# Performance work log

Measured on AMD Instinct MI355X. Metric: run time of the kernel, lower is better.

## Reference

```python
import jax, jax.numpy as jnp
import numpy as np

N_NODES = 100000
N_EDGES = 1600000
IN_DIM = 256
OUT_DIM = 32


def setup_inputs() -> dict:
    key = jax.random.key(0)
    k1, k2, k3, k4, k5 = jax.random.split(key, 5)
    x = jax.random.normal(k1, (N_NODES, IN_DIM), dtype=jnp.float32)
    src = jax.random.randint(k2, (N_EDGES,), 0, N_NODES, dtype=jnp.int32)
    dst = jax.random.randint(k3, (N_EDGES,), 0, N_NODES, dtype=jnp.int32)
    # GraphConv parameters (DGL: weight [in, out], bias [out])
    W = jax.random.normal(k4, (IN_DIM, OUT_DIM), dtype=jnp.float32) / np.sqrt(IN_DIM)
    b = jnp.zeros((OUT_DIM,), dtype=jnp.float32)
    return {"x": x, "src": src, "dst": dst, "W": W, "b": b}


def reference(x, src, dst, W, b):
    # DGL GraphConv, norm='both', allow_zero_in_degree=True:
    #   out = D_in^{-1/2} A D_out^{-1/2} X W + b  (degrees clamped to min 1)
    ones = jnp.ones(src.shape[0], dtype=x.dtype)
    deg_out = jax.ops.segment_sum(ones, src, num_segments=N_NODES)
    deg_in = jax.ops.segment_sum(ones, dst, num_segments=N_NODES)
    norm_src = jnp.clip(deg_out, 1.0, None) ** -0.5  # [N]
    norm_dst = jnp.clip(deg_in, 1.0, None) ** -0.5   # [N]
    # in_dim > out_dim: project first (smaller messages), then aggregate
    h = (x * norm_src[:, None]) @ W                  # [N, out]
    msgs = h[src]                                    # [E, out] gather
    agg = jax.ops.segment_sum(msgs, dst, num_segments=N_NODES)  # [N, out]
    return agg * norm_dst[:, None] + b
```

## Files before the change

### kernel.cpp

```cpp
#include <hip/hip_runtime.h>

#define N_NODES 100000
#define N_EDGES 1600000
#define IN_DIM 256
#define OUT_DIM 32

#define SB_SHIFT 7
#define NSB ((N_NODES + 127) >> 7)
#define SBCAP 2368
#define NB1 782
#define NGB ((N_NODES + 255) / 256)
#define NI4 (N_EDGES / 4)

typedef __attribute__((ext_vector_type(8))) short short8;
typedef __attribute__((ext_vector_type(16))) float f32x16;

#define WT_STRIDE 264

__device__ inline unsigned short f2bf(float f) {
    unsigned u = __float_as_uint(f);
    unsigned r = u + 0x7FFF + ((u >> 16) & 1);
    return (unsigned short)(r >> 16);
}
__device__ inline float bf2f(unsigned short us) {
    return __uint_as_float((unsigned)us << 16);
}

__global__ __launch_bounds__(512) void k_mega(const int* __restrict__ src,
                                              const int* __restrict__ dst,
                                              unsigned long long* __restrict__ qcnt,
                                              unsigned* __restrict__ gsb,
                                              unsigned char* __restrict__ gss,
                                              const float* __restrict__ x,
                                              const float* __restrict__ W,
                                              unsigned short* __restrict__ h2) {
    __shared__ __align__(16) int smemI[6 * NSB];
    const int tid = threadIdx.x;
    const int bid = blockIdx.x;
    const int g = bid / 3;
    const int rem = bid - g * 3;

    if (rem == 0) {
        unsigned short* WT = (unsigned short*)smemI;
        #pragma unroll
        for (int i = 0; i < 16; ++i) {
            int idx = tid + i * 512;
            WT[(idx & 31) * WT_STRIDE + (idx >> 5)] = f2bf(W[idx]);
        }
        __syncthreads();

        const int wv = tid >> 6;
        const int lane = tid & 63;
        const int col = lane & 31;
        const int hi = lane >> 5;

        const int row0 = g * 256 + wv * 32;
        int grow = row0 + col;
        int growc = grow < N_NODES ? grow : N_NODES - 1;
        const float4* xrow = reinterpret_cast<const float4*>(x + (size_t)growc * IN_DIM);

        f32x16 acc = {0.f,0.f,0.f,0.f,0.f,0.f,0.f,0.f,
                      0.f,0.f,0.f,0.f,0.f,0.f,0.f,0.f};

        #pragma unroll 4
        for (int t = 0; t < 16; ++t) {
            int k4 = t * 4 + hi * 2;
            float4 p0 = xrow[k4];
            float4 p1 = xrow[k4 + 1];
            short8 a;
            a[0] = (short)f2bf(p0.x); a[1] = (short)f2bf(p0.y);
            a[2] = (short)f2bf(p0.z); a[3] = (short)f2bf(p0.w);
            a[4] = (short)f2bf(p1.x); a[5] = (short)f2bf(p1.y);
            a[6] = (short)f2bf(p1.z); a[7] = (short)f2bf(p1.w);
            short8 bfr = *reinterpret_cast<const short8*>(
                &WT[col * WT_STRIDE + t * 16 + hi * 8]);
            acc = __builtin_amdgcn_mfma_f32_32x32x16_bf16(a, bfr, acc, 0, 0, 0);
        }

        #pragma unroll
        for (int r = 0; r < 16; ++r) {
            int rowi = (r & 3) + 8 * (r >> 2) + 4 * hi;
            int go = row0 + rowi;
            if (go < N_NODES)
                h2[(size_t)go * OUT_DIM + col] = f2bf(acc[r]);
        }
    } else {
        const int pb = 2 * g + rem - 1;
        int* histD = smemI;
        int* bbD   = smemI + NSB;
        int* curD  = smemI + 2 * NSB;
        int* histS = smemI + 3 * NSB;
        int* bbS   = smemI + 4 * NSB;
        int* curS  = smemI + 5 * NSB;

        for (int i = tid; i < NSB; i += 512) {
            histD[i] = 0; curD[i] = 0; histS[i] = 0; curS[i] = 0;
        }
        __syncthreads();

        const int gid = pb * 512 + tid;
        const bool valid = gid < NI4;
        int4 sv, dv;
        if (valid) {
            sv = reinterpret_cast<const int4*>(src)[gid];
            dv = reinterpret_cast<const int4*>(dst)[gid];
            atomicAdd(&histD[dv.x >> SB_SHIFT], 1);
            atomicAdd(&histD[dv.y >> SB_SHIFT], 1);
            atomicAdd(&histD[dv.z >> SB_SHIFT], 1);
            atomicAdd(&histD[dv.w >> SB_SHIFT], 1);
            atomicAdd(&histS[sv.x >> SB_SHIFT], 1);
            atomicAdd(&histS[sv.y >> SB_SHIFT], 1);
            atomicAdd(&histS[sv.z >> SB_SHIFT], 1);
            atomicAdd(&histS[sv.w >> SB_SHIFT], 1);
        }
        __syncthreads();

        for (int i = tid; i < NSB; i += 512) {
            unsigned long long pack =
                ((unsigned long long)(unsigned)histS[i] << 32) | (unsigned)histD[i];
            unsigned long long old = atomicAdd(&qcnt[i], pack);
            bbD[i] = (int)(old & 0xFFFFFFFFull);
            bbS[i] = (int)(old >> 32);
        }
        __syncthreads();

        if (valid) {
            int ss[4] = {sv.x, sv.y, sv.z, sv.w};
            int dd[4] = {dv.x, dv.y, dv.z, dv.w};
            #pragma unroll
            for (int u = 0; u < 4; ++u) {
                int d = dd[u], s = ss[u];
                int r = d >> SB_SHIFT;
                int lp = atomicAdd(&curD[r], 1);
                int pos = bbD[r] + lp;
                if (pos < SBCAP)
                    gsb[(size_t)r * SBCAP + pos] =
                        ((unsigned)(d & 127) << 17) | (unsigned)s;
                int rs = s >> SB_SHIFT;
                int lp2 = atomicAdd(&curS[rs], 1);
                int pos2 = bbS[rs] + lp2;
                if (pos2 < SBCAP)
                    gss[(size_t)rs * SBCAP + pos2] = (unsigned char)(s & 127);
            }
        }
    }
}

__global__ __launch_bounds__(256) void k_deg2(const int* __restrict__ qcnt2,
                                              const unsigned char* __restrict__ gss,
                                              float* __restrict__ nrmtab) {
    __shared__ int hist[128];
    const int r = blockIdx.x;
    const int tid = threadIdx.x;
    if (tid < 128) hist[tid] = 0;
    __syncthreads();
    int cnt = qcnt2[2 * r + 1];
    if (cnt > SBCAP) cnt = SBCAP;
    const unsigned char* bp = gss + (size_t)r * SBCAP;
    for (int i = tid; i < cnt; i += 256)
        atomicAdd(&hist[bp[i]], 1);
    __syncthreads();
    if (tid < 128) {
        int nn = (r << SB_SHIFT) + tid;
        if (nn < N_NODES) {
            int dg = hist[tid];
            nrmtab[nn] = rsqrtf((float)(dg > 1 ? dg : 1));
        }
    }
}

__global__ __launch_bounds__(512) void k_combo2(const int* __restrict__ qcnt2,
                                                const unsigned* __restrict__ gsb,
                                                const unsigned short* __restrict__ h2,
                                                const float* __restrict__ nrmtab,
                                                const float* __restrict__ bias,
                                                float* __restrict__ out) {
    __shared__ unsigned pstage[SBCAP];
    __shared__ int esl[SBCAP];
    __shared__ int hist[128];
    __shared__ int pref[128];
    __shared__ int cur[128];

    const int r = blockIdx.x;
    const int tid = threadIdx.x;

    if (tid < 128) { hist[tid] = 0; cur[tid] = 0; }
    int cnt = qcnt2[2 * r];
    if (cnt > SBCAP) cnt = SBCAP;
    const unsigned* bp = gsb + (size_t)r * SBCAP;
    __syncthreads();

    for (int i = tid; i < cnt; i += 512) {
        unsigned pay = bp[i];
        pstage[i] = pay;
        atomicAdd(&hist[pay >> 17], 1);
    }
    __syncthreads();

    int v = 0;
    if (tid < 128) { v = hist[tid]; pref[tid] = v; }
    __syncthreads();
    #pragma unroll
    for (int off = 1; off < 128; off <<= 1) {
        int t = (tid < 128 && tid >= off) ? pref[tid - off] : 0;
        __syncthreads();
        if (tid < 128) pref[tid] += t;
        __syncthreads();
    }
    if (tid < 128) pref[tid] -= v;
    __syncthreads();

    for (int i = tid; i < cnt; i += 512) {
        unsigned pay = pstage[i];
        int l = (int)(pay >> 17);
        int lp = atomicAdd(&cur[l], 1);
        esl[pref[l] + lp] = (int)(pay & 0x1FFFF);
    }
    __syncthreads();

    const int q = tid & 7;
    const int nl = tid >> 3;
    const float4 bb = reinterpret_cast<const float4*>(bias)[q];
    #pragma unroll
    for (int sweep = 0; sweep < 2; ++sweep) {
        int l = sweep * 64 + nl;
        int st = pref[l];
        int deg = hist[l];
        float4 acc = make_float4(0.f, 0.f, 0.f, 0.f);
        int j = 0;
        for (; j + 4 <= deg; j += 4) {
            int s0 = esl[st + j + 0];
            int s1 = esl[st + j + 1];
            int s2 = esl[st + j + 2];
            int s3 = esl[st + j + 3];
            float w0 = nrmtab[s0];
            float w1 = nrmtab[s1];
            float w2 = nrmtab[s2];
            float w3 = nrmtab[s3];
            ushort4 a0 = *reinterpret_cast<const ushort4*>(&h2[(size_t)s0 * OUT_DIM + q * 4]);
            ushort4 a1 = *reinterpret_cast<const ushort4*>(&h2[(size_t)s1 * OUT_DIM + q * 4]);
            ushort4 a2 = *reinterpret_cast<const ushort4*>(&h2[(size_t)s2 * OUT_DIM + q * 4]);
            ushort4 a3 = *reinterpret_cast<const ushort4*>(&h2[(size_t)s3 * OUT_DIM + q * 4]);
            acc.x += bf2f(a0.x) * w0 + bf2f(a1.x) * w1 + bf2f(a2.x) * w2 + bf2f(a3.x) * w3;
            acc.y += bf2f(a0.y) * w0 + bf2f(a1.y) * w1 + bf2f(a2.y) * w2 + bf2f(a3.y) * w3;
            acc.z += bf2f(a0.z) * w0 + bf2f(a1.z) * w1 + bf2f(a2.z) * w2 + bf2f(a3.z) * w3;
            acc.w += bf2f(a0.w) * w0 + bf2f(a1.w) * w1 + bf2f(a2.w) * w2 + bf2f(a3.w) * w3;
        }
        for (; j < deg; ++j) {
            int s = esl[st + j];
            float w = nrmtab[s];
            ushort4 a = *reinterpret_cast<const ushort4*>(&h2[(size_t)s * OUT_DIM + q * 4]);
            acc.x += bf2f(a.x) * w; acc.y += bf2f(a.y) * w;
            acc.z += bf2f(a.z) * w; acc.w += bf2f(a.w) * w;
        }
        int node = (r << SB_SHIFT) + l;
        if (node < N_NODES) {
            float nrm = rsqrtf((float)(deg > 1 ? deg : 1));
            float4 o = make_float4(acc.x * nrm + bb.x, acc.y * nrm + bb.y,
                                   acc.z * nrm + bb.z, acc.w * nrm + bb.w);
            reinterpret_cast<float4*>(out)[(size_t)node * 8 + q] = o;
        }
    }
}

extern "C" void kernel_launch(void* const* d_in, const int* in_sizes, int n_in,
                              void* d_out, int out_size, void* d_ws, size_t ws_size,
                              hipStream_t stream) {
    const float* x   = (const float*)d_in[0];
    const int*   src = (const int*)d_in[1];
    const int*   dst = (const int*)d_in[2];
    const float* W   = (const float*)d_in[3];
    const float* b   = (const float*)d_in[4];
    float* out = (float*)d_out;

    float* nrmtab = (float*)d_ws;
    unsigned long long* qcnt = (unsigned long long*)((char*)d_ws + 400000);
    int* qcnt2 = (int*)qcnt;
    unsigned short* h2 = (unsigned short*)((char*)d_ws + 406272);
    unsigned* gsb = (unsigned*)((char*)d_ws + 6806272);
    unsigned char* gss = (unsigned char*)((char*)d_ws + 14213376);

    hipMemsetAsync(qcnt, 0, NSB * sizeof(unsigned long long), stream);

    k_mega<<<NB1 + NGB, 512, 0, stream>>>(src, dst, qcnt, gsb, gss, x, W, h2);

    k_deg2<<<NSB, 256, 0, stream>>>(qcnt2, gss, nrmtab);

    k_combo2<<<NSB, 512, 0, stream>>>(qcnt2, gsb, h2, nrmtab, b, out);
}
```

Baseline: 90.12 us.

## Split fused partition/GEMM mega-kernel into separate kernels with prefetched x loads

Splits the heterogeneous mega-kernel, which interleaved edge-partition blocks with GEMM blocks, into two separate launches: an edge bucketing kernel and a dedicated bf16 MFMA projection kernel. The GEMM kernel now uses 256-thread blocks over 128 rows with less LDS, and software-prefetches x rows four steps ahead in registers. This is meant to improve occupancy and memory-level parallelism for the x stream. It gives up the concurrent overlap of the two workloads and adds a kernel launch.

```diff
diff --git a/kernel.cpp b/kernel.cpp
--- a/kernel.cpp
+++ b/kernel.cpp
@@ -9,7 +9,6 @@
 #define NSB ((N_NODES + 127) >> 7)
 #define SBCAP 2368
 #define NB1 782
-#define NGB ((N_NODES + 255) / 256)
 #define NI4 (N_EDGES / 4)
 
 typedef __attribute__((ext_vector_type(8))) short short8;
@@ -26,123 +25,130 @@
     return __uint_as_float((unsigned)us << 16);
 }
 
-__global__ __launch_bounds__(512) void k_mega(const int* __restrict__ src,
-                                              const int* __restrict__ dst,
-                                              unsigned long long* __restrict__ qcnt,
-                                              unsigned* __restrict__ gsb,
-                                              unsigned char* __restrict__ gss,
-                                              const float* __restrict__ x,
+__global__ __launch_bounds__(512) void k_part1(const int* __restrict__ src,
+                                               const int* __restrict__ dst,
+                                               unsigned long long* __restrict__ qcnt,
+                                               unsigned* __restrict__ gsb,
+                                               unsigned char* __restrict__ gss) {
+    __shared__ int smemI[6 * NSB];
+    const int tid = threadIdx.x;
+    int* histD = smemI;
+    int* bbD   = smemI + NSB;
+    int* curD  = smemI + 2 * NSB;
+    int* histS = smemI + 3 * NSB;
+    int* bbS   = smemI + 4 * NSB;
+    int* curS  = smemI + 5 * NSB;
+
+    for (int i = tid; i < NSB; i += 512) {
+        histD[i] = 0; curD[i] = 0; histS[i] = 0; curS[i] = 0;
+    }
+    __syncthreads();
+
+    const int gid = blockIdx.x * 512 + tid;
+    const bool valid = gid < NI4;
+    int4 sv, dv;
+    if (valid) {
+        sv = reinterpret_cast<const int4*>(src)[gid];
+        dv = reinterpret_cast<const int4*>(dst)[gid];
+        atomicAdd(&histD[dv.x >> SB_SHIFT], 1);
+        atomicAdd(&histD[dv.y >> SB_SHIFT], 1);
+        atomicAdd(&histD[dv.z >> SB_SHIFT], 1);
+        atomicAdd(&histD[dv.w >> SB_SHIFT], 1);
+        atomicAdd(&histS[sv.x >> SB_SHIFT], 1);
+        atomicAdd(&histS[sv.y >> SB_SHIFT], 1);
+        atomicAdd(&histS[sv.z >> SB_SHIFT], 1);
+        atomicAdd(&histS[sv.w >> SB_SHIFT], 1);
+    }
+    __syncthreads();
+
+    for (int i = tid; i < NSB; i += 512) {
+        unsigned long long pack =
+            ((unsigned long long)(unsigned)histS[i] << 32) | (unsigned)histD[i];
+        unsigned long long old = atomicAdd(&qcnt[i], pack);
+        bbD[i] = (int)(old & 0xFFFFFFFFull);
+        bbS[i] = (int)(old >> 32);
+    }
+    __syncthreads();
+
+    if (valid) {
+        int ss[4] = {sv.x, sv.y, sv.z, sv.w};
+        int dd[4] = {dv.x, dv.y, dv.z, dv.w};
+        #pragma unroll
+        for (int u = 0; u < 4; ++u) {
+            int d = dd[u], s = ss[u];
+            int r = d >> SB_SHIFT;
+            int lp = atomicAdd(&curD[r], 1);
+            int pos = bbD[r] + lp;
+            if (pos < SBCAP)
+                gsb[(size_t)r * SBCAP + pos] =
+                    ((unsigned)(d & 127) << 17) | (unsigned)s;
+            int rs = s >> SB_SHIFT;
+            int lp2 = atomicAdd(&curS[rs], 1);
+            int pos2 = bbS[rs] + lp2;
+            if (pos2 < SBCAP)
+                gss[(size_t)rs * SBCAP + pos2] = (unsigned char)(s & 127);
+        }
+    }
+}
+
+__global__ __launch_bounds__(256) void k_gemm(const float* __restrict__ x,
                                               const float* __restrict__ W,
                                               unsigned short* __restrict__ h2) {
-    __shared__ __align__(16) int smemI[6 * NSB];
-    const int tid = threadIdx.x;
-    const int bid = blockIdx.x;
-    const int g = bid / 3;
-    const int rem = bid - g * 3;
-
-    if (rem == 0) {
-        unsigned short* WT = (unsigned short*)smemI;
-        #pragma unroll
-        for (int i = 0; i < 16; ++i) {
-            int idx = tid + i * 512;
-            WT[(idx & 31) * WT_STRIDE + (idx >> 5)] = f2bf(W[idx]);
-        }
-        __syncthreads();
-
-        const int wv = tid >> 6;
-        const int lane = tid & 63;
-        const int col = lane & 31;
-        const int hi = lane >> 5;
-
-        const int row0 = g * 256 + wv * 32;
-        int grow = row0 + col;
-        int growc = grow < N_NODES ? grow : N_NODES - 1;
-        const float4* xrow = reinterpret_cast<const float4*>(x + (size_t)growc * IN_DIM);
-
-        f32x16 acc = {0.f,0.f,0.f,0.f,0.f,0.f,0.f,0.f,
-                      0.f,0.f,0.f,0.f,0.f,0.f,0.f,0.f};
-
-        #pragma unroll 4
-        for (int t = 0; t < 16; ++t) {
-            int k4 = t * 4 + hi * 2;
-            float4 p0 = xrow[k4];
-            float4 p1 = xrow[k4 + 1];
-            short8 a;
-            a[0] = (short)f2bf(p0.x); a[1] = (short)f2bf(p0.y);
-            a[2] = (short)f2bf(p0.z); a[3] = (short)f2bf(p0.w);
-            a[4] = (short)f2bf(p1.x); a[5] = (short)f2bf(p1.y);
-            a[6] = (short)f2bf(p1.z); a[7] = (short)f2bf(p1.w);
-            short8 bfr = *reinterpret_cast<const short8*>(
-                &WT[col * WT_STRIDE + t * 16 + hi * 8]);
-            acc = __builtin_amdgcn_mfma_f32_32x32x16_bf16(a, bfr, acc, 0, 0, 0);
-        }
-
-        #pragma unroll
-        for (int r = 0; r < 16; ++r) {
-            int rowi = (r & 3) + 8 * (r >> 2) + 4 * hi;
-            int go = row0 + rowi;
-            if (go < N_NODES)
-                h2[(size_t)go * OUT_DIM + col] = f2bf(acc[r]);
-        }
-    } else {
-        const int pb = 2 * g + rem - 1;
-        int* histD = smemI;
-        int* bbD   = smemI + NSB;
-        int* curD  = smemI + 2 * NSB;
-        int* histS = smemI + 3 * NSB;
-        int* bbS   = smemI + 4 * NSB;
-        int* curS  = smemI + 5 * NSB;
-
-        for (int i = tid; i < NSB; i += 512) {
-            histD[i] = 0; curD[i] = 0; histS[i] = 0; curS[i] = 0;
-        }
-        __syncthreads();
-
-        const int gid = pb * 512 + tid;
-        const bool valid = gid < NI4;
-        int4 sv, dv;
-        if (valid) {
-            sv = reinterpret_cast<const int4*>(src)[gid];
-            dv = reinterpret_cast<const int4*>(dst)[gid];
-            atomicAdd(&histD[dv.x >> SB_SHIFT], 1);
-            atomicAdd(&histD[dv.y >> SB_SHIFT], 1);
-            atomicAdd(&histD[dv.z >> SB_SHIFT], 1);
-            atomicAdd(&histD[dv.w >> SB_SHIFT], 1);
-            atomicAdd(&histS[sv.x >> SB_SHIFT], 1);
-            atomicAdd(&histS[sv.y >> SB_SHIFT], 1);
-            atomicAdd(&histS[sv.z >> SB_SHIFT], 1);
-            atomicAdd(&histS[sv.w >> SB_SHIFT], 1);
-        }
-        __syncthreads();
-
-        for (int i = tid; i < NSB; i += 512) {
-            unsigned long long pack =
-                ((unsigned long long)(unsigned)histS[i] << 32) | (unsigned)histD[i];
-            unsigned long long old = atomicAdd(&qcnt[i], pack);
-            bbD[i] = (int)(old & 0xFFFFFFFFull);
-            bbS[i] = (int)(old >> 32);
-        }
-        __syncthreads();
-
-        if (valid) {
-            int ss[4] = {sv.x, sv.y, sv.z, sv.w};
-            int dd[4] = {dv.x, dv.y, dv.z, dv.w};
-            #pragma unroll
-            for (int u = 0; u < 4; ++u) {
-                int d = dd[u], s = ss[u];
-                int r = d >> SB_SHIFT;
-                int lp = atomicAdd(&curD[r], 1);
-                int pos = bbD[r] + lp;
-                if (pos < SBCAP)
-                    gsb[(size_t)r * SBCAP + pos] =
-                        ((unsigned)(d & 127) << 17) | (unsigned)s;
-                int rs = s >> SB_SHIFT;
-                int lp2 = atomicAdd(&curS[rs], 1);
-                int pos2 = bbS[rs] + lp2;
-                if (pos2 < SBCAP)
-                    gss[(size_t)rs * SBCAP + pos2] = (unsigned char)(s & 127);
-            }
-        }
+    __shared__ unsigned short WT[32 * WT_STRIDE];
+
+    const int tid = threadIdx.x;
+    #pragma unroll
+    for (int i = 0; i < 32; ++i) {
+        int idx = tid + i * 256;
+        WT[(idx & 31) * WT_STRIDE + (idx >> 5)] = f2bf(W[idx]);
+    }
+    __syncthreads();
+
+    const int wv = tid >> 6;
+    const int lane = tid & 63;
+    const int col = lane & 31;
+    const int hi = lane >> 5;
+
+    const int row0 = blockIdx.x * 128 + wv * 32;
+    int grow = row0 + col;
+    int growc = grow < N_NODES ? grow : N_NODES - 1;
+    const float4* xrow = reinterpret_cast<const float4*>(x + (size_t)growc * IN_DIM);
+
+    f32x16 acc = {0.f,0.f,0.f,0.f,0.f,0.f,0.f,0.f,
+                  0.f,0.f,0.f,0.f,0.f,0.f,0.f,0.f};
+
+    float4 p0[4], p1[4];
+    #pragma unroll
+    for (int t = 0; t < 4; ++t) {
+        p0[t] = xrow[t * 4 + hi * 2];
+        p1[t] = xrow[t * 4 + hi * 2 + 1];
+    }
+
+    #pragma unroll
+    for (int t = 0; t < 16; ++t) {
+        const int sl = t & 3;
+        float4 q0 = p0[sl];
+        float4 q1 = p1[sl];
+        if (t + 4 < 16) {
+            p0[sl] = xrow[(t + 4) * 4 + hi * 2];
+            p1[sl] = xrow[(t + 4) * 4 + hi * 2 + 1];
+        }
+        short8 a;
+        a[0] = (short)f2bf(q0.x); a[1] = (short)f2bf(q0.y);
+        a[2] = (short)f2bf(q0.z); a[3] = (short)f2bf(q0.w);
+        a[4] = (short)f2bf(q1.x); a[5] = (short)f2bf(q1.y);
+        a[6] = (short)f2bf(q1.z); a[7] = (short)f2bf(q1.w);
+        short8 bfr = *reinterpret_cast<const short8*>(
+            &WT[col * WT_STRIDE + t * 16 + hi * 8]);
+        acc = __builtin_amdgcn_mfma_f32_32x32x16_bf16(a, bfr, acc, 0, 0, 0);
+    }
+
+    #pragma unroll
+    for (int r = 0; r < 16; ++r) {
+        int rowi = (r & 3) + 8 * (r >> 2) + 4 * hi;
+        int go = row0 + rowi;
+        if (go < N_NODES)
+            h2[(size_t)go * OUT_DIM + col] = f2bf(acc[r]);
     }
 }
 
@@ -282,7 +288,9 @@
 
     hipMemsetAsync(qcnt, 0, NSB * sizeof(unsigned long long), stream);
 
-    k_mega<<<NB1 + NGB, 512, 0, stream>>>(src, dst, qcnt, gsb, gss, x, W, h2);
+    k_part1<<<NB1, 512, 0, stream>>>(src, dst, qcnt, gsb, gss);
+
+    k_gemm<<<(N_NODES + 127) / 128, 256, 0, stream>>>(x, W, h2);
 
     k_deg2<<<NSB, 256, 0, stream>>>(qcnt2, gss, nrmtab);
 
```

Measured after the change: 115.6 us. 1.28x slower.
